# Performance work log

Measured on AMD Instinct MI355X. Metric: run time of the kernel, lower is better.

The kernel has to match this reference:

```python
import jax, jax.numpy as jnp
import numpy as np

N_USERS, N_ITEMS, N_TAGS = 20000, 20000, 5000
N_NODES = N_USERS + N_ITEMS + N_TAGS  # 45000
EMB = 64
N_HOPS = 2
E_RAND = 600000
E = E_RAND + N_NODES  # 645000 edges incl. self-loops (add_residual)


def _xavier(k, shape):
    a = float(np.sqrt(6.0 / (shape[0] + shape[1])))
    return jax.random.uniform(k, shape, jnp.float32, -a, a)


def setup_inputs() -> dict:
    key = jax.random.key(0)
    ks = jax.random.split(key, 10)
    # COO graph indices; self-loops appended as in Recommender.add_residual
    head = jnp.concatenate([jax.random.randint(ks[0], (E_RAND,), 0, N_NODES),
                            jnp.arange(N_NODES)]).astype(jnp.int32)
    tail = jnp.concatenate([jax.random.randint(ks[1], (E_RAND,), 0, N_NODES),
                            jnp.arange(N_NODES)]).astype(jnp.int32)
    return {
        "user_emb": jax.random.normal(ks[2], (N_USERS, EMB), jnp.float32),
        "user_offset_emb": jax.random.normal(ks[3], (N_USERS, EMB), jnp.float32),
        "item_emb": jax.random.normal(ks[4], (N_ITEMS, EMB), jnp.float32),
        "item_offset_emb": jax.random.normal(ks[5], (N_ITEMS, EMB), jnp.float32),
        "tag_emb": jax.random.normal(ks[6], (N_TAGS, EMB), jnp.float32),
        "tag_offset": jax.random.normal(ks[7], (N_TAGS, EMB), jnp.float32),
        "W1": _xavier(ks[8], (EMB, EMB)),
        "b1": jnp.zeros((EMB,), jnp.float32),
        "W2": _xavier(ks[9], (EMB, EMB)),
        "b2": jnp.zeros((EMB,), jnp.float32),
        "head": head,
        "tail": tail,
    }


def _seg_softmax(src, idx, n_seg):
    # scatter_softmax: per-segment, per-feature softmax over edges
    m = jax.ops.segment_max(src, idx, num_segments=n_seg)
    m = jnp.where(jnp.isfinite(m), m, 0.0)
    e = jnp.exp(src - m[idx])
    s = jax.ops.segment_sum(e, idx, num_segments=n_seg)
    return e / s[idx]


def _center_net(embs, idx, n_seg, W1, b1, W2, b2):
    # CenterIntersection: Linear->relu->Linear->scatter_softmax->weighted scatter_sum
    h = jax.nn.relu(embs @ W1.T + b1)
    a = h @ W2.T + b2
    attn = _seg_softmax(a, idx, n_seg)
    return jax.ops.segment_sum(attn * embs, idx, num_segments=n_seg)


def _masked_seg_reduce(src, idx, mask, n_seg, union):
    # BoxOffsetIntersection over an edge subset: route masked-out edges to a
    # dummy segment; empty segments become 0 (torch_scatter semantics).
    idx2 = jnp.where(mask, idx, n_seg)
    if union:
        out = jax.ops.segment_max(src, idx2, num_segments=n_seg + 1)[:n_seg]
    else:
        out = jax.ops.segment_min(src, idx2, num_segments=n_seg + 1)[:n_seg]
    return jnp.where(jnp.isfinite(out), out, 0.0)


def reference(user_emb, user_offset_emb, item_emb, item_offset_emb, tag_emb,
              tag_offset, W1, b1, W2, b2, head, tail):
    nu, ni = N_USERS, N_ITEMS
    all_embs = jnp.concatenate([user_emb, item_emb, tag_emb], axis=0)
    all_off = jax.nn.relu(jnp.concatenate([user_offset_emb, item_offset_emb, tag_offset], axis=0))
    m_iu = (head < nu) & (tail >= nu) & (tail < nu + ni)   # user<-item edges
    m_ut = (head < nu) & (tail >= nu + ni)                 # user<-tag edges
    m_it = (head >= nu) & (head < nu + ni)                 # item head edges
    m_tg = head >= nu + ni                                 # tag head edges
    for _ in range(N_HOPS):
        emb_e = all_embs[tail]                       # [E, d] gather
        agg_emb = _center_net(emb_e, head, N_NODES, W1, b1, W2, b2)
        off_e = jax.nn.relu(all_off[tail])           # [E, d]
        iu = _masked_seg_reduce(off_e, head, m_iu, N_NODES, union=False)[:nu]
        ut = _masked_seg_reduce(off_e, head, m_ut, N_NODES, union=True)[:nu]
        # union of the two user offsets via scatter_min over user_union_idx + relu
        user_off = jax.nn.relu(jnp.minimum(iu, ut))
        item_off = _masked_seg_reduce(off_e, head, m_it, N_NODES, union=True)[nu:nu + ni]
        tag_off = _masked_seg_reduce(off_e, head, m_tg, N_NODES, union=False)[nu + ni:]
        # F.normalize (L2, dim=1)
        agg_emb = agg_emb / jnp.maximum(
            jnp.linalg.norm(agg_emb, axis=1, keepdims=True), 1e-12)
        all_embs = agg_emb
        all_off = jax.nn.relu(jnp.concatenate([user_off, item_off, tag_off], axis=0))
    return (all_embs[:nu], all_off[:nu],
            all_embs[nu:nu + ni], all_off[nu:nu + ni],
            all_embs[nu + ni:], all_off[nu + ni:])
```

## Files before the change

### kernel.cpp

```cpp
#include <hip/hip_runtime.h>
#include <math.h>

#define NU 20000
#define NI 20000
#define NT 5000
#define NN 45000
#define D  64
#define CAP 64
#define MBLK 704

typedef unsigned short u16;
typedef unsigned int u32;

typedef __attribute__((ext_vector_type(8))) short bf16x8;
typedef __attribute__((ext_vector_type(4))) float f32x4;

__device__ __forceinline__ float b2f(u16 u) {
  return __uint_as_float(((u32)u) << 16);
}
__device__ __forceinline__ u16 f2b(float f) {
  u32 x = __float_as_uint(f);
  u32 r = (x + 0x7fffu + ((x >> 16) & 1u)) >> 16;
  return (u16)r;
}
__device__ __forceinline__ const float* row3(int n, const float* a, const float* b, const float* c) {
  if (n < NU) return a + (size_t)n * D;
  if (n < NU + NI) return b + (size_t)(n - NU) * D;
  return c + (size_t)(n - NU - NI) * D;
}
__device__ __forceinline__ bf16x8 cvtf8(const float* p) {
  bf16x8 r;
#pragma unroll
  for (int j = 0; j < 8; ++j) r[j] = (short)f2b(p[j]);
  return r;
}

template <int FIRST>
__device__ __forceinline__ void mlp_body(
    int bid,
    const float* __restrict__ ue, const float* __restrict__ ie, const float* __restrict__ te,
    const float* __restrict__ uo, const float* __restrict__ io, const float* __restrict__ to,
    const u16* __restrict__ Xc,
    const float* __restrict__ W1, const float* __restrict__ b1,
    const float* __restrict__ W2, const float* __restrict__ b2,
    u32* __restrict__ PE, u16* __restrict__ O1) {
  __shared__ u16 W1L[64][72];
  __shared__ u16 W2L[64][72];
  __shared__ u16 Hs[64][72];
  int tid = threadIdx.x;
  for (int i = tid; i < 4096; i += 256) {
    W1L[i >> 6][i & 63] = f2b(W1[i]);
    W2L[i >> 6][i & 63] = f2b(W2[i]);
  }
  __syncthreads();
  int w = tid >> 6, l = tid & 63;
  int lr = l & 15, kh = l >> 4;
  int nbase = bid * 64 + w * 16;
  int na = nbase + lr; if (na > NN - 1) na = NN - 1;
  bf16x8 A0, A1;
  if (FIRST) {
    const float* xr = row3(na, ue, ie, te);
    A0 = cvtf8(xr + kh * 8);
    A1 = cvtf8(xr + 32 + kh * 8);
  } else {
    A0 = *(const bf16x8*)(Xc + (size_t)na * 64 + kh * 8);
    A1 = *(const bf16x8*)(Xc + (size_t)na * 64 + 32 + kh * 8);
  }
#pragma unroll
  for (int ft = 0; ft < 4; ++ft) {
    int f = ft * 16 + lr;
    bf16x8 Bl = *(const bf16x8*)&W1L[f][kh * 8];
    bf16x8 Bh = *(const bf16x8*)&W1L[f][32 + kh * 8];
    f32x4 z = {0.f, 0.f, 0.f, 0.f};
    z = __builtin_amdgcn_mfma_f32_16x16x32_bf16(A0, Bl, z, 0, 0, 0);
    z = __builtin_amdgcn_mfma_f32_16x16x32_bf16(A1, Bh, z, 0, 0, 0);
    float bb = b1[f];
#pragma unroll
    for (int r = 0; r < 4; ++r)
      Hs[w * 16 + kh * 4 + r][f] = f2b(fmaxf(z[r] + bb, 0.f));
  }
  __syncthreads();
  bf16x8 A20 = *(const bf16x8*)&Hs[w * 16 + lr][kh * 8];
  bf16x8 A21 = *(const bf16x8*)&Hs[w * 16 + lr][32 + kh * 8];
#pragma unroll
  for (int ft = 0; ft < 4; ++ft) {
    int f = ft * 16 + lr;
    bf16x8 Bl = *(const bf16x8*)&W2L[f][kh * 8];
    bf16x8 Bh = *(const bf16x8*)&W2L[f][32 + kh * 8];
    f32x4 z = {0.f, 0.f, 0.f, 0.f};
    z = __builtin_amdgcn_mfma_f32_16x16x32_bf16(A20, Bl, z, 0, 0, 0);
    z = __builtin_amdgcn_mfma_f32_16x16x32_bf16(A21, Bh, z, 0, 0, 0);
    float bb = b2[f];
#pragma unroll
    for (int r = 0; r < 4; ++r) {
      int node = nbase + kh * 4 + r;
      if (node < NN) {
        float a = z[r] + bb;
        float p = __expf(fminf(fmaxf(a, -60.f), 60.f));
        u32 idx = ((u32)node << 6) + f;
        u32 eb;
        if (FIRST) {
          eb = f2b(row3(node, ue, ie, te)[f]);
          O1[idx] = f2b(fmaxf(row3(node, uo, io, to)[f], 0.f));
        } else {
          eb = Xc[idx];
        }
        PE[idx] = (u32)f2b(p) | (eb << 16);
      }
    }
  }
}

__global__ __launch_bounds__(256) void fused1_kernel(
    const float* __restrict__ ue, const float* __restrict__ ie, const float* __restrict__ te,
    const float* __restrict__ uo, const float* __restrict__ io, const float* __restrict__ to,
    const float* __restrict__ W1, const float* __restrict__ b1,
    const float* __restrict__ W2, const float* __restrict__ b2,
    const int* __restrict__ head, const int* __restrict__ tail, int ER,
    u32* __restrict__ PE, u16* __restrict__ O1,
    int* __restrict__ cnt, u16* __restrict__ csr) {
  int bid = blockIdx.x;
  if (bid >= MBLK) {
    int i = (bid - MBLK) * 256 + threadIdx.x;
    if (i < ER) {
      int h = head[i];
      int s = atomicAdd(&cnt[h], 1);
      if (s < CAP) csr[h * CAP + s] = (u16)tail[i];
    }
    return;
  }
  mlp_body<1>(bid, ue, ie, te, uo, io, to, nullptr, W1, b1, W2, b2, PE, O1);
}

__global__ __launch_bounds__(256) void mlp2_kernel(
    const u16* __restrict__ Xc,
    const float* __restrict__ W1, const float* __restrict__ b1,
    const float* __restrict__ W2, const float* __restrict__ b2,
    u32* __restrict__ PE) {
  mlp_body<0>(blockIdx.x, nullptr, nullptr, nullptr, nullptr, nullptr, nullptr,
              Xc, W1, b1, W2, b2, PE, nullptr);
}

template <int FINAL>
__global__ __launch_bounds__(256) void agg_kernel(
    const int* __restrict__ cnt, const u16* __restrict__ csr,
    const u32* __restrict__ PE, const u16* __restrict__ O,
    u16* __restrict__ Xco, u16* __restrict__ Oo, float* __restrict__ out) {
  int n = (blockIdx.x * blockDim.x + threadIdx.x) >> 6;
  int lane = threadIdx.x & 63;
  if (n >= NN) return;
  int cn = min(cnt[n], CAP);
  int tl = (lane < cn) ? (int)csr[n * CAP + lane] : 0;
  u32 vs = PE[((u32)n << 6) + lane];
  float ps = b2f((u16)(vs & 0xffffu));
  float es = b2f((u16)(vs >> 16));
  float os = b2f(O[((u32)n << 6) + lane]);
  float ss0 = ps, ss1 = 0.f, ss2 = 0.f, ss3 = 0.f;
  float ts0 = ps * es, ts1 = 0.f, ts2 = 0.f, ts3 = 0.f;
  float mn0 = 3.4e38f, mn1 = 3.4e38f;
  float mx0 = -3.4e38f, mx1 = -3.4e38f;
  if (n >= NU) {
    if (n < NU + NI) mx0 = os;
    else             mn0 = os;
  }

#define LDP(T) PE[((u32)(T) << 6) + lane]
#define LDO(T) O[((u32)(T) << 6) + lane]
#define ACC(V, SS, TS)                                  \
  { float p_ = b2f((u16)((V) & 0xffffu));               \
    float e_ = b2f((u16)((V) >> 16));                   \
    SS += p_; TS = fmaf(p_, e_, TS); }

  if (n < NU) {
    int j = 0;
    for (; j + 7 < cn; j += 8) {
      int t0 = __shfl(tl, j),     t1 = __shfl(tl, j + 1);
      int t2 = __shfl(tl, j + 2), t3 = __shfl(tl, j + 3);
      int t4 = __shfl(tl, j + 4), t5 = __shfl(tl, j + 5);
      int t6 = __shfl(tl, j + 6), t7 = __shfl(tl, j + 7);
      u32 v0 = LDP(t0), v1 = LDP(t1), v2 = LDP(t2), v3 = LDP(t3);
      u32 v4 = LDP(t4), v5 = LDP(t5), v6 = LDP(t6), v7 = LDP(t7);
      float o0 = b2f(LDO(t0)), o1 = b2f(LDO(t1)), o2 = b2f(LDO(t2)), o3 = b2f(LDO(t3));
      float o4 = b2f(LDO(t4)), o5 = b2f(LDO(t5)), o6 = b2f(LDO(t6)), o7 = b2f(LDO(t7));
      ACC(v0, ss0, ts0) ACC(v1, ss1, ts1) ACC(v2, ss2, ts2) ACC(v3, ss3, ts3)
      ACC(v4, ss0, ts0) ACC(v5, ss1, ts1) ACC(v6, ss2, ts2) ACC(v7, ss3, ts3)
      if (t0 >= NU + NI) mx0 = fmaxf(mx0, o0); else if (t0 >= NU) mn0 = fminf(mn0, o0);
      if (t1 >= NU + NI) mx1 = fmaxf(mx1, o1); else if (t1 >= NU) mn1 = fminf(mn1, o1);
      if (t2 >= NU + NI) mx0 = fmaxf(mx0, o2); else if (t2 >= NU) mn0 = fminf(mn0, o2);
      if (t3 >= NU + NI) mx1 = fmaxf(mx1, o3); else if (t3 >= NU) mn1 = fminf(mn1, o3);
      if (t4 >= NU + NI) mx0 = fmaxf(mx0, o4); else if (t4 >= NU) mn0 = fminf(mn0, o4);
      if (t5 >= NU + NI) mx1 = fmaxf(mx1, o5); else if (t5 >= NU) mn1 = fminf(mn1, o5);
      if (t6 >= NU + NI) mx0 = fmaxf(mx0, o6); else if (t6 >= NU) mn0 = fminf(mn0, o6);
      if (t7 >= NU + NI) mx1 = fmaxf(mx1, o7); else if (t7 >= NU) mn1 = fminf(mn1, o7);
    }
    for (; j < cn; ++j) {
      int t = __shfl(tl, j);
      u32 v = LDP(t);
      float o = b2f(LDO(t));
      ACC(v, ss0, ts0)
      if (t >= NU + NI) mx0 = fmaxf(mx0, o); else if (t >= NU) mn0 = fminf(mn0, o);
    }
  } else if (n < NU + NI) {
    int j = 0;
    for (; j + 7 < cn; j += 8) {
      int t0 = __shfl(tl, j),     t1 = __shfl(tl, j + 1);
      int t2 = __shfl(tl, j + 2), t3 = __shfl(tl, j + 3);
      int t4 = __shfl(tl, j + 4), t5 = __shfl(tl, j + 5);
      int t6 = __shfl(tl, j + 6), t7 = __shfl(tl, j + 7);
      u32 v0 = LDP(t0), v1 = LDP(t1), v2 = LDP(t2), v3 = LDP(t3);
      u32 v4 = LDP(t4), v5 = LDP(t5), v6 = LDP(t6), v7 = LDP(t7);
      float o0 = b2f(LDO(t0)), o1 = b2f(LDO(t1)), o2 = b2f(LDO(t2)), o3 = b2f(LDO(t3));
      float o4 = b2f(LDO(t4)), o5 = b2f(LDO(t5)), o6 = b2f(LDO(t6)), o7 = b2f(LDO(t7));
      ACC(v0, ss0, ts0) ACC(v1, ss1, ts1) ACC(v2, ss2, ts2) ACC(v3, ss3, ts3)
      ACC(v4, ss0, ts0) ACC(v5, ss1, ts1) ACC(v6, ss2, ts2) ACC(v7, ss3, ts3)
      mx0 = fmaxf(mx0, o0); mx1 = fmaxf(mx1, o1);
      mx0 = fmaxf(mx0, o2); mx1 = fmaxf(mx1, o3);
      mx0 = fmaxf(mx0, o4); mx1 = fmaxf(mx1, o5);
      mx0 = fmaxf(mx0, o6); mx1 = fmaxf(mx1, o7);
    }
    for (; j < cn; ++j) {
      int t = __shfl(tl, j);
      u32 v = LDP(t);
      float o = b2f(LDO(t));
      ACC(v, ss0, ts0)
      mx0 = fmaxf(mx0, o);
    }
  } else {
    int j = 0;
    for (; j + 7 < cn; j += 8) {
      int t0 = __shfl(tl, j),     t1 = __shfl(tl, j + 1);
      int t2 = __shfl(tl, j + 2), t3 = __shfl(tl, j + 3);
      int t4 = __shfl(tl, j + 4), t5 = __shfl(tl, j + 5);
      int t6 = __shfl(tl, j + 6), t7 = __shfl(tl, j + 7);
      u32 v0 = LDP(t0), v1 = LDP(t1), v2 = LDP(t2), v3 = LDP(t3);
      u32 v4 = LDP(t4), v5 = LDP(t5), v6 = LDP(t6), v7 = LDP(t7);
      float o0 = b2f(LDO(t0)), o1 = b2f(LDO(t1)), o2 = b2f(LDO(t2)), o3 = b2f(LDO(t3));
      float o4 = b2f(LDO(t4)), o5 = b2f(LDO(t5)), o6 = b2f(LDO(t6)), o7 = b2f(LDO(t7));
      ACC(v0, ss0, ts0) ACC(v1, ss1, ts1) ACC(v2, ss2, ts2) ACC(v3, ss3, ts3)
      ACC(v4, ss0, ts0) ACC(v5, ss1, ts1) ACC(v6, ss2, ts2) ACC(v7, ss3, ts3)
      mn0 = fminf(mn0, o0); mn1 = fminf(mn1, o1);
      mn0 = fminf(mn0, o2); mn1 = fminf(mn1, o3);
      mn0 = fminf(mn0, o4); mn1 = fminf(mn1, o5);
      mn0 = fminf(mn0, o6); mn1 = fminf(mn1, o7);
    }
    for (; j < cn; ++j) {
      int t = __shfl(tl, j);
      u32 v = LDP(t);
      float o = b2f(LDO(t));
      ACC(v, ss0, ts0)
      mn0 = fminf(mn0, o);
    }
  }
#undef LDP
#undef LDO
#undef ACC

  float ssum = (ss0 + ss1) + (ss2 + ss3);
  float tsum = (ts0 + ts1) + (ts2 + ts3);
  float omin = fminf(mn0, mn1), omax = fmaxf(mx0, mx1);
  float agg = tsum / ssum;
  float sq = agg * agg;
#pragma unroll
  for (int msk = 1; msk < 64; msk <<= 1) sq += __shfl_xor(sq, msk);
  float outv = agg / fmaxf(sqrtf(sq), 1e-12f);
  float offv;
  if (n < NU) {
    float iu = (omin > 1e37f) ? 0.f : omin;
    float ut = (omax < -1e37f) ? 0.f : omax;
    offv = fmaxf(fminf(iu, ut), 0.f);
  } else if (n < NU + NI) {
    offv = fmaxf((omax < -1e37f) ? 0.f : omax, 0.f);
  } else {
    offv = fmaxf((omin > 1e37f) ? 0.f : omin, 0.f);
  }
  if (FINAL) {
    float* oe; float* oo;
    if (n < NU)           { oe = out + (size_t)n * D;
                            oo = out + (size_t)NU * D + (size_t)n * D; }
    else if (n < NU + NI) { int q = n - NU;
                            oe = out + (size_t)2 * NU * D + (size_t)q * D;
                            oo = oe + (size_t)NI * D; }
    else                  { int q = n - NU - NI;
                            oe = out + (size_t)(2 * NU + 2 * NI) * D + (size_t)q * D;
                            oo = oe + (size_t)NT * D; }
    __builtin_nontemporal_store(outv, &oe[lane]);
    __builtin_nontemporal_store(offv, &oo[lane]);
  } else {
    u32 idx = ((u32)n << 6) + lane;
    Xco[idx] = f2b(outv);
    Oo[idx] = f2b(offv);
  }
}

extern "C" void kernel_launch(void* const* d_in, const int* in_sizes, int n_in,
                              void* d_out, int out_size, void* d_ws, size_t ws_size,
                              hipStream_t stream) {
  const float* ue = (const float*)d_in[0];
  const float* uo = (const float*)d_in[1];
  const float* ie = (const float*)d_in[2];
  const float* io = (const float*)d_in[3];
  const float* te = (const float*)d_in[4];
  const float* to = (const float*)d_in[5];
  const float* W1 = (const float*)d_in[6];
  const float* b1 = (const float*)d_in[7];
  const float* W2 = (const float*)d_in[8];
  const float* b2 = (const float*)d_in[9];
  const int* head = (const int*)d_in[10];
  const int* tail = (const int*)d_in[11];
  int E = in_sizes[10];
  int ER = E - NN;

  const size_t NE = (size_t)NN * 64;
  u32* PE  = (u32*)d_ws;
  u16* O1  = (u16*)(PE + NE);
  u16* O2  = O1 + NE;
  u16* Xc  = O2 + NE;
  int* cnt = (int*)(Xc + NE);
  u16* csr = (u16*)(cnt + NN);

  hipMemsetAsync(cnt, 0, NN * sizeof(int), stream);
  int nsb = (ER + 255) / 256;

  fused1_kernel<<<MBLK + nsb, 256, 0, stream>>>(
      ue, ie, te, uo, io, to, W1, b1, W2, b2, head, tail, ER, PE, O1, cnt, csr);
  int ab = (NN + 3) / 4;
  agg_kernel<0><<<ab, 256, 0, stream>>>(cnt, csr, PE, O1, Xc, O2, nullptr);

  mlp2_kernel<<<MBLK, 256, 0, stream>>>(Xc, W1, b1, W2, b2, PE);
  agg_kernel<1><<<ab, 256, 0, stream>>>(cnt, csr, PE, O2, nullptr, nullptr, (float*)d_out);
}
```

Measured before the change: 142.4 us.

## Pre-partition edges by head range so CSR atomics stay XCD-local

Adds a partition pass that buckets edges into eight head-node ranges, packing head and tail into a single 32-bit word. The CSR-build blocks are then interleaved so each bucket maps to one XCD, on the assumption that blocks are dispatched round-robin across XCDs. The goal is to keep the atomicAdd traffic on cnt and the csr writes in one XCD's L2 and cut cross-die coherence traffic. The cost is an extra kernel launch and an extra pass over the edge list. It also relies on the fixed BCAP bucket capacity, so edges past that limit are silently dropped.

After: 166.4 us. +16.8%, slower.

```diff
diff --git a/kernel.cpp b/kernel.cpp
--- a/kernel.cpp
+++ b/kernel.cpp
@@ -8,6 +8,9 @@
 #define D  64
 #define CAP 64
 #define MBLK 704
+#define NXCD 8
+#define HRANGE 5625
+#define BCAP 80000
 
 typedef unsigned short u16;
 typedef unsigned int u32;
@@ -33,6 +36,31 @@
 #pragma unroll
   for (int j = 0; j < 8; ++j) r[j] = (short)f2b(p[j]);
   return r;
+}
+
+__global__ __launch_bounds__(256) void part_kernel(
+    const int* __restrict__ head, const int* __restrict__ tail, int ER,
+    int* __restrict__ bcnt, u32* __restrict__ pk) {
+  __shared__ int lcnt[NXCD];
+  __shared__ int lbase[NXCD];
+  int tid = threadIdx.x;
+  if (tid < NXCD) lcnt[tid] = 0;
+  __syncthreads();
+  int i = blockIdx.x * 256 + tid;
+  int b = -1, h = 0, t = 0, pos = 0;
+  if (i < ER) {
+    h = head[i];
+    t = tail[i];
+    b = h / HRANGE;
+    pos = atomicAdd(&lcnt[b], 1);
+  }
+  __syncthreads();
+  if (tid < NXCD) lbase[tid] = atomicAdd(&bcnt[tid], lcnt[tid]);
+  __syncthreads();
+  if (b >= 0) {
+    int idx = lbase[b] + pos;
+    if (idx < BCAP) pk[b * BCAP + idx] = ((u32)h << 16) | (u32)t;
+  }
 }
 
 template <int FIRST>
@@ -116,16 +144,21 @@
     const float* __restrict__ uo, const float* __restrict__ io, const float* __restrict__ to,
     const float* __restrict__ W1, const float* __restrict__ b1,
     const float* __restrict__ W2, const float* __restrict__ b2,
-    const int* __restrict__ head, const int* __restrict__ tail, int ER,
+    const int* __restrict__ bcnt, const u32* __restrict__ pk,
     u32* __restrict__ PE, u16* __restrict__ O1,
     int* __restrict__ cnt, u16* __restrict__ csr) {
   int bid = blockIdx.x;
   if (bid >= MBLK) {
-    int i = (bid - MBLK) * 256 + threadIdx.x;
-    if (i < ER) {
-      int h = head[i];
+    int sbid = bid - MBLK;
+    int p = sbid & (NXCD - 1);
+    int chunk = sbid >> 3;
+    int cp = min(bcnt[p], BCAP);
+    int i = chunk * 256 + threadIdx.x;
+    if (i < cp) {
+      u32 e = pk[p * BCAP + i];
+      int h = e >> 16;
       int s = atomicAdd(&cnt[h], 1);
-      if (s < CAP) csr[h * CAP + s] = (u16)tail[i];
+      if (s < CAP) csr[h * CAP + s] = (u16)(e & 0xffffu);
     }
     return;
   }
@@ -316,13 +349,18 @@
   u16* O2  = O1 + NE;
   u16* Xc  = O2 + NE;
   int* cnt = (int*)(Xc + NE);
-  u16* csr = (u16*)(cnt + NN);
-
-  hipMemsetAsync(cnt, 0, NN * sizeof(int), stream);
-  int nsb = (ER + 255) / 256;
-
+  int* bcnt = cnt + NN;
+  u16* csr = (u16*)(bcnt + NXCD);
+  u32* pk  = (u32*)(csr + (size_t)NN * CAP);
+
+  hipMemsetAsync(cnt, 0, (NN + NXCD) * sizeof(int), stream);
+  int npb = (ER + 255) / 256;
+
+  part_kernel<<<npb, 256, 0, stream>>>(head, tail, ER, bcnt, pk);
+
+  int nsb = NXCD * ((BCAP + 255) / 256);
   fused1_kernel<<<MBLK + nsb, 256, 0, stream>>>(
-      ue, ie, te, uo, io, to, W1, b1, W2, b2, head, tail, ER, PE, O1, cnt, csr);
+      ue, ie, te, uo, io, to, W1, b1, W2, b2, bcnt, pk, PE, O1, cnt, csr);
   int ab = (NN + 3) / 4;
   agg_kernel<0><<<ab, 256, 0, stream>>>(cnt, csr, PE, O1, Xc, O2, nullptr);
 
```
